# Kernel tuning notes

Measured on AMD Instinct MI355X. Metric: run time of the kernel, lower is better.

## Reference

```python
import jax, jax.numpy as jnp
import numpy as np

NUM_Q_HEADS = 32
NUM_KV_HEADS = 8
HEAD_DIM = 128
HIDDEN = 4096
MAX_WAVELENGTH = 10000.0
ROPE_SCALING = 1.0


def apply_rope(x, start_index=0):
    # x: [b, s, h, d]; keras_hub RotaryEmbedding: concat-half (NeoX/Llama) style
    s, d = x.shape[1], x.shape[3]
    inv_freq = 1.0 / (MAX_WAVELENGTH ** (jnp.arange(0, d, 2, dtype=jnp.float32) / d))
    pos = (jnp.arange(s, dtype=jnp.float32) + start_index) / ROPE_SCALING
    freq = pos[:, None] * inv_freq[None, :]           # [s, d/2]
    emb = jnp.concatenate([freq, freq], axis=-1)      # [s, d]
    cos = jnp.cos(emb)[None, :, None, :]
    sin = jnp.sin(emb)[None, :, None, :]
    x1, x2 = jnp.split(x, 2, axis=-1)
    half_rot = jnp.concatenate([-x2, x1], axis=-1)
    return x * cos + half_rot * sin


def setup_inputs() -> dict:
    key = jax.random.key(0)
    k1, k2, k3, k4, k5 = jax.random.split(key, 5)
    B, S = 1, 2048
    hidden_states = jax.random.normal(k1, (B, S, HIDDEN), dtype=jnp.float32)
    # causal mask [B, q, k]
    attention_mask = jnp.broadcast_to(jnp.tril(jnp.ones((S, S), dtype=bool)), (B, S, S))
    scale = 1.0 / np.sqrt(HIDDEN)
    wq = jax.random.normal(k2, (HIDDEN, NUM_Q_HEADS, HEAD_DIM), dtype=jnp.float32) * scale
    wk = jax.random.normal(k3, (HIDDEN, NUM_KV_HEADS, HEAD_DIM), dtype=jnp.float32) * scale
    wv = jax.random.normal(k4, (HIDDEN, NUM_KV_HEADS, HEAD_DIM), dtype=jnp.float32) * scale
    wo = jax.random.normal(k5, (NUM_Q_HEADS, HEAD_DIM, HIDDEN), dtype=jnp.float32) * scale
    return {"hidden_states": hidden_states, "attention_mask": attention_mask,
            "wq": wq, "wk": wk, "wv": wv, "wo": wo}


def reference(hidden_states, attention_mask, wq, wk, wv, wo):
    groups = NUM_Q_HEADS // NUM_KV_HEADS
    norm = jnp.sqrt(jnp.asarray(HEAD_DIM, dtype=hidden_states.dtype))
    query = jnp.einsum('bqm,muh->bquh', hidden_states, wq)   # [b,q,Hq,d]
    key = jnp.einsum('bkm,mvh->bkvh', hidden_states, wk)     # [b,k,Hkv,d]
    value = jnp.einsum('bkm,mvh->bkvh', hidden_states, wv)
    query = apply_rope(query)
    key = apply_rope(key)
    # repeat KV heads for GQA (ops.repeat on head axis)
    key = jnp.repeat(key, groups, axis=2)
    value = jnp.repeat(value, groups, axis=2)
    scores = jnp.einsum('bquh,bkuh->buqk', query, key) / norm  # [b,H,q,k]
    scores = scores.astype(jnp.float32)
    scores = jnp.where(attention_mask[:, None, :, :], scores, jnp.float32(-1e9))
    probs = jax.nn.softmax(scores, axis=-1).astype(hidden_states.dtype)
    attn = jnp.einsum('buqk,bkuh->bquh', probs, value)
    out = jnp.einsum('bquh,uhm->bqm', attn, wo)
    return out
```

## Files before the change

### kernel.cpp

```cpp
#include <hip/hip_runtime.h>
#include <hip/hip_bf16.h>
#include <stdint.h>

#define S_LEN 2048
#define HID 4096
#define NQH 32
#define NKVH 8
#define HD 128
#define QKV_LD 6144

typedef __attribute__((ext_vector_type(8))) short bf16x8;
typedef __attribute__((ext_vector_type(4))) float f32x4;
typedef __attribute__((address_space(3))) uint8_t lds_u8_t;
typedef __attribute__((address_space(1))) uint8_t glb_u8_t;

__device__ __forceinline__ void g2lds16(const void* g, void* l) {
  __builtin_amdgcn_global_load_lds((const glb_u8_t*)g, (lds_u8_t*)l, 16, 0, 0);
}

__device__ __forceinline__ ushort f2bf(float x) {
  return __builtin_bit_cast(ushort, __float2bfloat16(x));
}
__device__ __forceinline__ float bf2f(ushort x) {
  return __bfloat162float(__builtin_bit_cast(__hip_bfloat16, x));
}

__device__ __forceinline__ void hard_barrier() {
  __builtin_amdgcn_sched_barrier(0);
  __builtin_amdgcn_s_barrier();
  __builtin_amdgcn_sched_barrier(0);
}

__global__ void k_f32_to_bf16(const float* __restrict__ in, ushort* __restrict__ out, int n4) {
  int i = blockIdx.x * blockDim.x + threadIdx.x;
  if (i >= n4) return;
  float4 v = ((const float4*)in)[i];
  ushort4 o;
  o.x = f2bf(v.x); o.y = f2bf(v.y); o.z = f2bf(v.z); o.w = f2bf(v.w);
  ((ushort4*)out)[i] = o;
}

__global__ void k_transpose_f32_bf16(const float* __restrict__ in, ushort* __restrict__ out,
                                     int ldi, int ldo) {
  __shared__ float tile[32][33];
  int j0 = blockIdx.x * 32, i0 = blockIdx.y * 32;
  int tx = threadIdx.x, ty = threadIdx.y;
#pragma unroll
  for (int k = 0; k < 4; ++k)
    tile[ty + 8 * k][tx] = in[(size_t)(i0 + ty + 8 * k) * ldi + j0 + tx];
  __syncthreads();
#pragma unroll
  for (int k = 0; k < 4; ++k)
    out[(size_t)(j0 + ty + 8 * k) * ldo + i0 + tx] = f2bf(tile[tx][ty + 8 * k]);
}

__global__ void k_transpose_bf16_head(const ushort* __restrict__ in, ushort* __restrict__ out) {
  __shared__ ushort tile[32][33];
  int hkv = blockIdx.z;
  int j0 = blockIdx.x * 32;
  int i0 = blockIdx.y * 32;
  const ushort* ih = in + hkv * HD;
  ushort* oh = out + (size_t)hkv * HD * S_LEN;
  int tx = threadIdx.x, ty = threadIdx.y;
#pragma unroll
  for (int k = 0; k < 4; ++k)
    tile[ty + 8 * k][tx] = ih[(size_t)(i0 + ty + 8 * k) * QKV_LD + j0 + tx];
  __syncthreads();
#pragma unroll
  for (int k = 0; k < 4; ++k)
    oh[(size_t)(j0 + ty + 8 * k) * S_LEN + i0 + tx] = tile[tx][ty + 8 * k];
}

__global__ void k_rope(ushort* __restrict__ X, int H, int logH, int ld, float mul) {
  int t = blockIdx.x * 256 + threadIdx.x;
  int d = t & 63;
  int rest = t >> 6;
  int h = rest & (H - 1);
  int s = rest >> logH;
  size_t base = (size_t)s * ld + h * HD + d;
  float inv = exp2f(-(float)d * 0.20762050593046014f);
  float fr = (float)s * inv;
  float c = cosf(fr), sn = sinf(fr);
  float x1 = bf2f(X[base]);
  float x2 = bf2f(X[base + 64]);
  X[base]      = f2bf((x1 * c - x2 * sn) * mul);
  X[base + 64] = f2bf((x2 * c + x1 * sn) * mul);
}

template <int OUT_BF16>
__global__ __launch_bounds__(512, 2) void k_gemm256(const ushort* __restrict__ A,
                                                    const ushort* __restrict__ BT,
                                                    void* __restrict__ Cv, int K, int ldc) {
  __shared__ char smem[131072];
  const int tid = threadIdx.x;
  const int lane = tid & 63, wave = tid >> 6;
  const int lo = lane & 15, hi = lane >> 4;
  const int wm = wave >> 2, wn = wave & 3;
  const int m0 = blockIdx.y * 256, n0 = blockIdx.x * 256;
  const int NT = K >> 5;

  const int src_cb = (((lane & 3) ^ ((lane >> 2) & 3)) << 4);
  const int rd_cb = ((hi ^ (lo & 3)) << 4);
  const int srow = wave * 16 + (lane >> 2);

  const char* Ab = (const char*)A;
  const char* Bb = (const char*)BT;

  const f32x4 z4 = {0.f, 0.f, 0.f, 0.f};
  f32x4 acc[8][4];
#pragma unroll
  for (int m = 0; m < 8; ++m)
#pragma unroll
    for (int n = 0; n < 4; ++n) acc[m][n] = z4;

  auto burst = [&](int u) {
    char* base = smem + (u & 3) * 32768;
    size_t k0b = (size_t)(u << 5) * 2;
#pragma unroll
    for (int i = 0; i < 2; ++i) {
      int r = srow + i * 128;
      g2lds16(Ab + (size_t)(m0 + r) * K * 2 + k0b + src_cb, base + i * 8192 + wave * 1024);
      g2lds16(Bb + (size_t)(n0 + r) * K * 2 + k0b + src_cb, base + 16384 + i * 8192 + wave * 1024);
    }
  };

  auto step = [&](int j) {
    const char* SA = smem + (j & 3) * 32768;
    const char* SB = SA + 16384;
    bf16x8 a[8], b[4];
#pragma unroll
    for (int m = 0; m < 4; ++m)
      a[m] = *(const bf16x8*)(SA + (wm * 128 + m * 16 + lo) * 64 + rd_cb);
#pragma unroll
    for (int n = 0; n < 4; ++n)
      b[n] = *(const bf16x8*)(SB + (wn * 64 + n * 16 + lo) * 64 + rd_cb);
    __builtin_amdgcn_s_setprio(1);
#pragma unroll
    for (int m = 0; m < 4; ++m)
#pragma unroll
      for (int n = 0; n < 4; ++n)
        acc[m][n] = __builtin_amdgcn_mfma_f32_16x16x32_bf16(a[m], b[n], acc[m][n], 0, 0, 0);
    __builtin_amdgcn_s_setprio(0);
#pragma unroll
    for (int m = 4; m < 8; ++m)
      a[m] = *(const bf16x8*)(SA + (wm * 128 + m * 16 + lo) * 64 + rd_cb);
    __builtin_amdgcn_s_setprio(1);
#pragma unroll
    for (int m = 4; m < 8; ++m)
#pragma unroll
      for (int n = 0; n < 4; ++n)
        acc[m][n] = __builtin_amdgcn_mfma_f32_16x16x32_bf16(a[m], b[n], acc[m][n], 0, 0, 0);
    __builtin_amdgcn_s_setprio(0);
  };

  burst(0); burst(1); burst(2);
  asm volatile("s_waitcnt vmcnt(8)" ::: "memory");
  hard_barrier();

  int j = 0;
  for (; j < NT - 3; ++j) {
    burst(j + 3);
    step(j);
    asm volatile("s_waitcnt vmcnt(8)" ::: "memory");
    hard_barrier();
  }
  step(j);
  asm volatile("s_waitcnt vmcnt(4)" ::: "memory");
  hard_barrier();
  ++j;
  step(j);
  asm volatile("s_waitcnt vmcnt(0)" ::: "memory");
  hard_barrier();
  ++j;
  step(j);

#pragma unroll
  for (int m = 0; m < 8; ++m)
#pragma unroll
    for (int n = 0; n < 4; ++n)
#pragma unroll
      for (int r = 0; r < 4; ++r) {
        int row = m0 + wm * 128 + m * 16 + 4 * hi + r;
        int col = n0 + wn * 64 + n * 16 + lo;
        if (OUT_BF16) {
          ((ushort*)Cv)[(size_t)row * ldc + col] = f2bf(acc[m][n][r]);
        } else {
          ((float*)Cv)[(size_t)row * ldc + col] = acc[m][n][r];
        }
      }
}

__global__ __launch_bounds__(256) void k_attn(const ushort* __restrict__ Q,
                                              const ushort* __restrict__ Kg,
                                              const ushort* __restrict__ VT,
                                              ushort* __restrict__ Ob) {
  __shared__ char smem[2 * 16384 + 2 * 16384 + 9216];
  int tid = threadIdx.x, lane = tid & 63, wave = tid >> 6;
  int hi = lane >> 4, lo = lane & 15;
  int h = blockIdx.y;
  int hkv = h >> 2;
  char* Pw = smem + 65536 + wave * 2304;
  const f32x4 z4 = {0.f, 0.f, 0.f, 0.f};
  bf16x8 ones;
#pragma unroll
  for (int i = 0; i < 8; ++i) ones[i] = (short)0x3F80;

  int L = wave * 4096 + lane * 16;
  int krow0 = L >> 8, kcolb = L & 255;
  int vrow0 = L >> 7, vcolb = L & 127;

#pragma unroll 1
  for (int pp = 0; pp < 2; ++pp) {
    int qt = pp == 0 ? (int)blockIdx.x : 31 - (int)blockIdx.x;
    int q0 = qt * 64;

    bf16x8 qf[4];
    const char* qrow = (const char*)Q + ((size_t)(q0 + 16 * wave + lo) * QKV_LD + h * HD) * 2;
#pragma unroll
    for (int c = 0; c < 4; ++c) qf[c] = *(const bf16x8*)(qrow + c * 64 + hi * 16);

    f32x4 oacc[8];
#pragma unroll
    for (int dg = 0; dg < 8; ++dg) oacc[dg] = z4;
    f32x4 lacc = z4;

#pragma unroll
    for (int j = 0; j < 4; ++j) {
      int kr = krow0 + j * 4, vr = vrow0 + j * 8;
      int ksrc = kcolb ^ ((kr & 7) << 4);
      int vsrc = vcolb ^ ((vr & 7) << 4);
      g2lds16((const char*)Kg + ((size_t)kr * QKV_LD + hkv * HD) * 2 + ksrc,
              smem + wave * 4096 + j * 1024);
      g2lds16((const char*)VT + ((size_t)(hkv * HD + vr) * S_LEN) * 2 + vsrc,
              smem + 32768 + wave * 4096 + j * 1024);
    }
    __syncthreads();

    for (int t = 0; t <= qt; ++t) {
      int cur = t & 1;
      char* Ks = smem + cur * 16384;
      char* Vs = smem + 32768 + cur * 16384;
      if (t < qt) {
        int kv1 = (t + 1) * 64;
        char* Kn = smem + (cur ^ 1) * 16384;
        char* Vn = smem + 32768 + (cur ^ 1) * 16384;
#pragma unroll
        for (int j = 0; j < 4; ++j) {
          int kr = krow0 + j * 4, vr = vrow0 + j * 8;
          int ksrc = kcolb ^ ((kr & 7) << 4);
          int vsrc = vcolb ^ ((vr & 7) << 4);
          g2lds16((const char*)Kg + ((size_t)(kv1 + kr) * QKV_LD + hkv * HD) * 2 + ksrc,
                  Kn + wave * 4096 + j * 1024);
          g2lds16((const char*)VT + ((size_t)(hkv * HD + vr) * S_LEN + kv1) * 2 + vsrc,
                  Vn + wave * 4096 + j * 1024);
        }
      }
      int kv0 = t * 64;

      f32x4 sg[4];
#pragma unroll
      for (int g = 0; g < 4; ++g) {
        f32x4 s = z4;
#pragma unroll
        for (int c = 0; c < 4; ++c) {
          int row = 16 * g + lo;
          int cb = (c * 64 + hi * 16) ^ ((row & 7) << 4);
          bf16x8 kf = *(const bf16x8*)(Ks + row * 256 + cb);
          s = __builtin_amdgcn_mfma_f32_16x16x32_bf16(qf[c], kf, s, 0, 0, 0);
        }
        sg[g] = s;
      }

      float pvv[4][4];
      if (t < qt) {
#pragma unroll
        for (int g = 0; g < 4; ++g)
#pragma unroll
          for (int r = 0; r < 4; ++r) pvv[g][r] = exp2f(sg[g][r]);
      } else {
#pragma unroll
        for (int g = 0; g < 4; ++g) {
          int kv_idx = kv0 + 16 * g + lo;
#pragma unroll
          for (int r = 0; r < 4; ++r) {
            int q_idx = q0 + 16 * wave + 4 * hi + r;
            float v = sg[g][r];
            if (kv_idx > q_idx) v = -1e30f;
            pvv[g][r] = exp2f(v);
          }
        }
      }

      {
        ushort* Pu = (ushort*)Pw;
#pragma unroll
        for (int g = 0; g < 4; ++g)
#pragma unroll
          for (int r = 0; r < 4; ++r)
            Pu[(4 * hi + r) * 72 + 16 * g + lo] = f2bf(pvv[g][r]);
      }
      asm volatile("" ::: "memory");

      bf16x8 pa[2];
#pragma unroll
      for (int c2 = 0; c2 < 2; ++c2)
        pa[c2] = *(const bf16x8*)(Pw + lo * 144 + c2 * 64 + hi * 16);
#pragma unroll
      for (int c2 = 0; c2 < 2; ++c2)
        lacc = __builtin_amdgcn_mfma_f32_16x16x32_bf16(pa[c2], ones, lacc, 0, 0, 0);
#pragma unroll
      for (int dg = 0; dg < 8; ++dg) {
#pragma unroll
        for (int c2 = 0; c2 < 2; ++c2) {
          int row = 16 * dg + lo;
          int cb = (c2 * 64 + hi * 16) ^ ((row & 7) << 4);
          bf16x8 vf = *(const bf16x8*)(Vs + row * 128 + cb);
          oacc[dg] = __builtin_amdgcn_mfma_f32_16x16x32_bf16(pa[c2], vf, oacc[dg], 0, 0, 0);
        }
      }
      __syncthreads();
    }

#pragma unroll
    for (int r = 0; r < 4; ++r) {
      float inv_l = 1.0f / lacc[r];
      int q = q0 + 16 * wave + 4 * hi + r;
      ushort* orow = Ob + (size_t)q * HID + h * HD;
#pragma unroll
      for (int dg = 0; dg < 8; ++dg)
        orow[16 * dg + lo] = f2bf(oacc[dg][r] * inv_l);
    }
  }
}

extern "C" void kernel_launch(void* const* d_in, const int* in_sizes, int n_in,
                              void* d_out, int out_size, void* d_ws, size_t ws_size,
                              hipStream_t stream) {
  const float* hidden = (const float*)d_in[0];
  const float* wq = (const float*)d_in[2];
  const float* wk = (const float*)d_in[3];
  const float* wv = (const float*)d_in[4];
  const float* wo = (const float*)d_in[5];

  char* ws = (char*)d_ws;
  ushort* hid_bf = (ushort*)(ws);
  ushort* wqkvT  = (ushort*)(ws + 16777216);
  ushort* VT     = (ushort*)(ws + 67108864);

  ushort* QKV = (ushort*)d_out;
  float* out = (float*)d_out;

  const float qmul = (float)(0.08838834764831845 * 1.4426950408889634);

  dim3 tb(32, 8);
  k_f32_to_bf16<<<8192, 256, 0, stream>>>(hidden, hid_bf, 2097152);
  k_transpose_f32_bf16<<<dim3(128, 128), tb, 0, stream>>>(wq, wqkvT, 4096, 4096);
  k_transpose_f32_bf16<<<dim3(32, 128), tb, 0, stream>>>(wk, wqkvT + (size_t)4096 * 4096, 1024, 4096);
  k_transpose_f32_bf16<<<dim3(32, 128), tb, 0, stream>>>(wv, wqkvT + (size_t)5120 * 4096, 1024, 4096);
  k_gemm256<1><<<dim3(24, 8), 512, 0, stream>>>(hid_bf, wqkvT, (void*)QKV, 4096, QKV_LD);
  k_rope<<<16384, 256, 0, stream>>>(QKV, 32, 5, QKV_LD, qmul);
  k_rope<<<4096, 256, 0, stream>>>(QKV + 4096, 8, 3, QKV_LD, 1.0f);
  k_transpose_bf16_head<<<dim3(4, 64, 8), tb, 0, stream>>>(QKV + 5120, VT);
  k_transpose_f32_bf16<<<dim3(128, 128), tb, 0, stream>>>(wo, wqkvT, 4096, 4096);
  k_attn<<<dim3(16, 32), 256, 0, stream>>>(QKV, QKV + 4096, VT, hid_bf);
  k_gemm256<0><<<dim3(16, 8), 512, 0, stream>>>(hid_bf, wqkvT, (void*)out, 4096, 4096);
}
```

Before: 513.1 us.

## Rewrite GEMM as 8-phase double-buffered pipeline with split-K for output projection

Replaces the 4-stage 32-wide K pipeline GEMM with a 64-wide K tile, double-buffered kernel. It interleaves LDS reads, global-to-LDS staging and MFMA bursts in four phases separated by barriers. The output projection now uses split-K across two z-slices so that 256 blocks run instead of 128. The second partial is stored in bf16 and added back by a new elementwise kernel. This adds an extra pass over the output and costs some precision on half of the K-sum.

```diff
diff --git a/kernel.cpp b/kernel.cpp
--- a/kernel.cpp
+++ b/kernel.cpp
@@ -38,6 +38,15 @@
   ushort4 o;
   o.x = f2bf(v.x); o.y = f2bf(v.y); o.z = f2bf(v.z); o.w = f2bf(v.w);
   ((ushort4*)out)[i] = o;
+}
+
+__global__ void k_sum_bf16(float* __restrict__ out, const ushort* __restrict__ p1, int n4) {
+  int i = blockIdx.x * blockDim.x + threadIdx.x;
+  if (i >= n4) return;
+  float4 a = ((float4*)out)[i];
+  ushort4 b = ((const ushort4*)p1)[i];
+  a.x += bf2f(b.x); a.y += bf2f(b.y); a.z += bf2f(b.z); a.w += bf2f(b.w);
+  ((float4*)out)[i] = a;
 }
 
 __global__ void k_transpose_f32_bf16(const float* __restrict__ in, ushort* __restrict__ out,
@@ -87,24 +96,36 @@
   X[base + 64] = f2bf((x2 * c + x1 * sn) * mul);
 }
 
-template <int OUT_BF16>
-__global__ __launch_bounds__(512, 2) void k_gemm256(const ushort* __restrict__ A,
-                                                    const ushort* __restrict__ BT,
-                                                    void* __restrict__ Cv, int K, int ldc) {
+template <int OUT_MODE>
+__global__ __launch_bounds__(512, 2) void k_gemm8p(const ushort* __restrict__ A,
+                                                   const ushort* __restrict__ BT,
+                                                   void* __restrict__ C0,
+                                                   void* __restrict__ C1,
+                                                   int Kstride, int NT, int ldc) {
   __shared__ char smem[131072];
-  const int tid = threadIdx.x;
-  const int lane = tid & 63, wave = tid >> 6;
+  const int tid = threadIdx.x, lane = tid & 63, wave = tid >> 6;
   const int lo = lane & 15, hi = lane >> 4;
   const int wm = wave >> 2, wn = wave & 3;
   const int m0 = blockIdx.y * 256, n0 = blockIdx.x * 256;
-  const int NT = K >> 5;
-
-  const int src_cb = (((lane & 3) ^ ((lane >> 2) & 3)) << 4);
-  const int rd_cb = ((hi ^ (lo & 3)) << 4);
-  const int srow = wave * 16 + (lane >> 2);
-
-  const char* Ab = (const char*)A;
-  const char* Bb = (const char*)BT;
+  const int kbase = blockIdx.z * NT * 64;
+  const size_t rowB = (size_t)Kstride * 2;
+
+  const int srccol = (((lane & 7) ^ ((lane >> 3) & 7)) << 4);
+  const char* srcA0 = (const char*)A + (size_t)(m0 + wave * 8 + (lane >> 3)) * rowB +
+                      (size_t)kbase * 2 + srccol;
+  const char* srcB0 = (const char*)BT + (size_t)(n0 + wave * 8 + (lane >> 3)) * rowB +
+                      (size_t)kbase * 2 + srccol;
+  const int rdx = (lo & 7) << 4;
+  const int kx0 = (hi * 16) ^ rdx;
+  const int kx1 = (64 + hi * 16) ^ rdx;
+  const int aBase = wm * 16384 + lo * 128;
+  const int bBase = 32768 + (wn * 64 + lo) * 128;
+
+  auto stage = [&](int t, int isB, int hq64, int ldsoff) {
+    const char* src = (isB ? srcB0 : srcA0) + (size_t)hq64 * rowB + (size_t)t * 128;
+    char* dst = smem + (t & 1) * 65536 + ldsoff + wave * 1024;
+    g2lds16(src, dst);
+  };
 
   const f32x4 z4 = {0.f, 0.f, 0.f, 0.f};
   f32x4 acc[8][4];
@@ -113,67 +134,105 @@
 #pragma unroll
     for (int n = 0; n < 4; ++n) acc[m][n] = z4;
 
-  auto burst = [&](int u) {
-    char* base = smem + (u & 3) * 32768;
-    size_t k0b = (size_t)(u << 5) * 2;
-#pragma unroll
-    for (int i = 0; i < 2; ++i) {
-      int r = srow + i * 128;
-      g2lds16(Ab + (size_t)(m0 + r) * K * 2 + k0b + src_cb, base + i * 8192 + wave * 1024);
-      g2lds16(Bb + (size_t)(n0 + r) * K * 2 + k0b + src_cb, base + 16384 + i * 8192 + wave * 1024);
-    }
-  };
-
-  auto step = [&](int j) {
-    const char* SA = smem + (j & 3) * 32768;
-    const char* SB = SA + 16384;
-    bf16x8 a[8], b[4];
+  stage(0, 0, 0, 0);       stage(0, 0, 128, 16384);
+  stage(0, 1, 0, 32768);   stage(0, 1, 64, 40960);
+  stage(0, 1, 128, 49152); stage(0, 1, 192, 57344);
+  stage(0, 0, 64, 8192);   stage(0, 0, 192, 24576);
+  stage(1, 0, 0, 0);       stage(1, 0, 128, 16384);
+  stage(1, 1, 0, 32768);   stage(1, 1, 64, 40960);
+  stage(1, 1, 128, 49152); stage(1, 1, 192, 57344);
+  asm volatile("s_waitcnt vmcnt(6)" ::: "memory");
+  hard_barrier();
+
+  bf16x8 aR[4][2], b01[2][2], b23[2][2];
+
+#pragma unroll 1
+  for (int t = 0; t < NT; ++t) {
+    const char* db = smem + (t & 1) * 65536;
+#pragma unroll
+    for (int m = 0; m < 4; ++m) {
+      aR[m][0] = *(const bf16x8*)(db + aBase + m * 2048 + kx0);
+      aR[m][1] = *(const bf16x8*)(db + aBase + m * 2048 + kx1);
+    }
+#pragma unroll
+    for (int n = 0; n < 2; ++n) {
+      b01[n][0] = *(const bf16x8*)(db + bBase + n * 2048 + kx0);
+      b01[n][1] = *(const bf16x8*)(db + bBase + n * 2048 + kx1);
+    }
+    if (t + 1 < NT) { stage(t + 1, 0, 64, 8192); stage(t + 1, 0, 192, 24576); }
+    hard_barrier();
+    asm volatile("s_waitcnt lgkmcnt(0)" ::: "memory");
+    __builtin_amdgcn_sched_barrier(0);
+    __builtin_amdgcn_s_setprio(1);
 #pragma unroll
     for (int m = 0; m < 4; ++m)
-      a[m] = *(const bf16x8*)(SA + (wm * 128 + m * 16 + lo) * 64 + rd_cb);
-#pragma unroll
-    for (int n = 0; n < 4; ++n)
-      b[n] = *(const bf16x8*)(SB + (wn * 64 + n * 16 + lo) * 64 + rd_cb);
+#pragma unroll
+      for (int n = 0; n < 2; ++n) {
+        acc[m][n] = __builtin_amdgcn_mfma_f32_16x16x32_bf16(aR[m][0], b01[n][0], acc[m][n], 0, 0, 0);
+        acc[m][n] = __builtin_amdgcn_mfma_f32_16x16x32_bf16(aR[m][1], b01[n][1], acc[m][n], 0, 0, 0);
+      }
+    __builtin_amdgcn_s_setprio(0);
+    hard_barrier();
+
+#pragma unroll
+    for (int n = 0; n < 2; ++n) {
+      b23[n][0] = *(const bf16x8*)(db + bBase + (n + 2) * 2048 + kx0);
+      b23[n][1] = *(const bf16x8*)(db + bBase + (n + 2) * 2048 + kx1);
+    }
+    if (t + 2 < NT) { stage(t + 2, 0, 0, 0); stage(t + 2, 0, 128, 16384); }
+    hard_barrier();
+    asm volatile("s_waitcnt lgkmcnt(0)" ::: "memory");
+    __builtin_amdgcn_sched_barrier(0);
     __builtin_amdgcn_s_setprio(1);
 #pragma unroll
     for (int m = 0; m < 4; ++m)
 #pragma unroll
-      for (int n = 0; n < 4; ++n)
-        acc[m][n] = __builtin_amdgcn_mfma_f32_16x16x32_bf16(a[m], b[n], acc[m][n], 0, 0, 0);
+      for (int n = 0; n < 2; ++n) {
+        acc[m][n + 2] = __builtin_amdgcn_mfma_f32_16x16x32_bf16(aR[m][0], b23[n][0], acc[m][n + 2], 0, 0, 0);
+        acc[m][n + 2] = __builtin_amdgcn_mfma_f32_16x16x32_bf16(aR[m][1], b23[n][1], acc[m][n + 2], 0, 0, 0);
+      }
     __builtin_amdgcn_s_setprio(0);
-#pragma unroll
-    for (int m = 4; m < 8; ++m)
-      a[m] = *(const bf16x8*)(SA + (wm * 128 + m * 16 + lo) * 64 + rd_cb);
+    hard_barrier();
+
+#pragma unroll
+    for (int m = 0; m < 4; ++m) {
+      aR[m][0] = *(const bf16x8*)(db + aBase + (m + 4) * 2048 + kx0);
+      aR[m][1] = *(const bf16x8*)(db + aBase + (m + 4) * 2048 + kx1);
+    }
+    if (t + 2 < NT) { stage(t + 2, 1, 0, 32768); stage(t + 2, 1, 64, 40960); }
+    hard_barrier();
+    asm volatile("s_waitcnt lgkmcnt(0)" ::: "memory");
+    __builtin_amdgcn_sched_barrier(0);
     __builtin_amdgcn_s_setprio(1);
 #pragma unroll
-    for (int m = 4; m < 8; ++m)
-#pragma unroll
-      for (int n = 0; n < 4; ++n)
-        acc[m][n] = __builtin_amdgcn_mfma_f32_16x16x32_bf16(a[m], b[n], acc[m][n], 0, 0, 0);
+    for (int m = 0; m < 4; ++m)
+#pragma unroll
+      for (int n = 0; n < 2; ++n) {
+        acc[m + 4][n + 2] = __builtin_amdgcn_mfma_f32_16x16x32_bf16(aR[m][0], b23[n][0], acc[m + 4][n + 2], 0, 0, 0);
+        acc[m + 4][n + 2] = __builtin_amdgcn_mfma_f32_16x16x32_bf16(aR[m][1], b23[n][1], acc[m + 4][n + 2], 0, 0, 0);
+      }
     __builtin_amdgcn_s_setprio(0);
-  };
-
-  burst(0); burst(1); burst(2);
-  asm volatile("s_waitcnt vmcnt(8)" ::: "memory");
-  hard_barrier();
-
-  int j = 0;
-  for (; j < NT - 3; ++j) {
-    burst(j + 3);
-    step(j);
-    asm volatile("s_waitcnt vmcnt(8)" ::: "memory");
+    hard_barrier();
+
+    if (t + 2 < NT) { stage(t + 2, 1, 128, 49152); stage(t + 2, 1, 192, 57344); }
+    hard_barrier();
+    __builtin_amdgcn_s_setprio(1);
+#pragma unroll
+    for (int m = 0; m < 4; ++m)
+#pragma unroll
+      for (int n = 0; n < 2; ++n) {
+        acc[m + 4][n] = __builtin_amdgcn_mfma_f32_16x16x32_bf16(aR[m][0], b01[n][0], acc[m + 4][n], 0, 0, 0);
+        acc[m + 4][n] = __builtin_amdgcn_mfma_f32_16x16x32_bf16(aR[m][1], b01[n][1], acc[m + 4][n], 0, 0, 0);
+      }
+    __builtin_amdgcn_s_setprio(0);
+    if (t < NT - 2)
+      asm volatile("s_waitcnt vmcnt(6)" ::: "memory");
+    else if (t == NT - 2)
+      asm volatile("s_waitcnt vmcnt(0)" ::: "memory");
     hard_barrier();
   }
-  step(j);
-  asm volatile("s_waitcnt vmcnt(4)" ::: "memory");
-  hard_barrier();
-  ++j;
-  step(j);
-  asm volatile("s_waitcnt vmcnt(0)" ::: "memory");
-  hard_barrier();
-  ++j;
-  step(j);
-
+
+  const int zz = blockIdx.z;
 #pragma unroll
   for (int m = 0; m < 8; ++m)
 #pragma unroll
@@ -182,10 +241,12 @@
       for (int r = 0; r < 4; ++r) {
         int row = m0 + wm * 128 + m * 16 + 4 * hi + r;
         int col = n0 + wn * 64 + n * 16 + lo;
-        if (OUT_BF16) {
-          ((ushort*)Cv)[(size_t)row * ldc + col] = f2bf(acc[m][n][r]);
+        float v = acc[m][n][r];
+        if (OUT_MODE == 0) {
+          ((ushort*)C0)[(size_t)row * ldc + col] = f2bf(v);
         } else {
-          ((float*)Cv)[(size_t)row * ldc + col] = acc[m][n][r];
+          if (zz == 0) ((float*)C0)[(size_t)row * ldc + col] = v;
+          else         ((ushort*)C1)[(size_t)row * ldc + col] = f2bf(v);
         }
       }
 }
@@ -345,9 +406,11 @@
   char* ws = (char*)d_ws;
   ushort* hid_bf = (ushort*)(ws);
   ushort* wqkvT  = (ushort*)(ws + 16777216);
-  ushort* VT     = (ushort*)(ws + 67108864);
-
+  ushort* Cpart1 = (ushort*)(ws + 50331648);
+
+  char* outc = (char*)d_out;
   ushort* QKV = (ushort*)d_out;
+  ushort* VT  = (ushort*)(outc + 25165824);
   float* out = (float*)d_out;
 
   const float qmul = (float)(0.08838834764831845 * 1.4426950408889634);
@@ -357,11 +420,12 @@
   k_transpose_f32_bf16<<<dim3(128, 128), tb, 0, stream>>>(wq, wqkvT, 4096, 4096);
   k_transpose_f32_bf16<<<dim3(32, 128), tb, 0, stream>>>(wk, wqkvT + (size_t)4096 * 4096, 1024, 4096);
   k_transpose_f32_bf16<<<dim3(32, 128), tb, 0, stream>>>(wv, wqkvT + (size_t)5120 * 4096, 1024, 4096);
-  k_gemm256<1><<<dim3(24, 8), 512, 0, stream>>>(hid_bf, wqkvT, (void*)QKV, 4096, QKV_LD);
+  k_gemm8p<0><<<dim3(24, 8, 1), 512, 0, stream>>>(hid_bf, wqkvT, (void*)QKV, nullptr, 4096, 64, QKV_LD);
   k_rope<<<16384, 256, 0, stream>>>(QKV, 32, 5, QKV_LD, qmul);
   k_rope<<<4096, 256, 0, stream>>>(QKV + 4096, 8, 3, QKV_LD, 1.0f);
   k_transpose_bf16_head<<<dim3(4, 64, 8), tb, 0, stream>>>(QKV + 5120, VT);
   k_transpose_f32_bf16<<<dim3(128, 128), tb, 0, stream>>>(wo, wqkvT, 4096, 4096);
   k_attn<<<dim3(16, 32), 256, 0, stream>>>(QKV, QKV + 4096, VT, hid_bf);
-  k_gemm256<0><<<dim3(16, 8), 512, 0, stream>>>(hid_bf, wqkvT, (void*)out, 4096, 4096);
-}
+  k_gemm8p<1><<<dim3(16, 8, 2), 512, 0, stream>>>(hid_bf, wqkvT, (void*)out, (void*)Cpart1, 4096, 32, 4096);
+  k_sum_bf16<<<8192, 256, 0, stream>>>(out, Cpart1, 2097152);
+}
```

Result: faster. 489.8 us (-4.5%).
